# Optimization experiments

Measured on AMD Instinct MI355X. Metric: run time of the kernel, lower is better.

## Reference

```python
import jax, jax.numpy as jnp
import numpy as np

B, N, F_, H, K_IN, K = 2, 768, 128, 128, 2, 2
TAU = 0.66


def setup_inputs() -> dict:
    key = jax.random.key(0)
    ks = jax.random.split(key, 8)
    s = lambda fan: 1.0 / np.sqrt(fan)
    X = jax.random.normal(ks[0], (B, N, F_), jnp.float32)
    # edge_feat RezeroMLP: Linear(F,H) -> act -> Linear(H,H)
    ef_w1 = jax.random.normal(ks[1], (F_, H), jnp.float32) * s(F_)
    ef_b1 = jnp.zeros((H,), jnp.float32)
    ef_w2 = jax.random.normal(ks[2], (H, H), jnp.float32) * s(H)
    ef_b2 = jnp.zeros((H,), jnp.float32)
    # rezero gate (init 0 in module; use small nonzero so the branch is exercised)
    gate = jnp.asarray(0.1, jnp.float32)
    # score_mlp RezeroMLP: Linear(k_in,H) -> ReLU -> Linear(H,k)
    sm_w1 = jax.random.normal(ks[3], (K_IN, H), jnp.float32) * s(K_IN)
    sm_b1 = jnp.zeros((H,), jnp.float32)
    sm_w2 = jax.random.normal(ks[4], (H, K), jnp.float32) * s(H)
    sm_b2 = jnp.zeros((K,), jnp.float32)
    # pre-sampled standard Gumbel noise for gumbel_softmax
    u = jax.random.uniform(ks[5], (B, N, N, K), jnp.float32, minval=1e-6, maxval=1.0 - 1e-6)
    gumbel = -jnp.log(-jnp.log(u))
    return {"X": X, "ef_w1": ef_w1, "ef_b1": ef_b1, "ef_w2": ef_w2, "ef_b2": ef_b2,
            "gate": gate, "sm_w1": sm_w1, "sm_b1": sm_b1, "sm_w2": sm_w2, "sm_b2": sm_b2,
            "gumbel": gumbel}


def reference(X, ef_w1, ef_b1, ef_w2, ef_b2, gate, sm_w1, sm_b1, sm_w2, sm_b2, gumbel):
    # edge_feat MLP: [B,N,F] -> [B,N,H]
    feats = jax.nn.relu(X @ ef_w1 + ef_b1) @ ef_w2 + ef_b2
    D = H // K_IN
    Xact = feats.reshape(B, N, D, K_IN)
    Xskip = X.reshape(B, N, D, K_IN)  # feat_dim == hidden_dim, proj is None
    Xc = (Xskip + gate * Xact).transpose(0, 3, 1, 2)  # [B,k_in,N,D]
    # pairwise outer product ('prod' scoring): [B,N,N,k_in]
    prod = jnp.einsum('bkid,bkjd->bijk', Xc, Xc)
    # per-edge score MLP: k_in -> H -> k
    scores = jax.nn.relu(prod @ sm_w1 + sm_b1) @ sm_w2 + sm_b2  # [B,N,N,k]
    logits = scores - jnp.max(scores, axis=-1, keepdims=True)
    # gumbel-softmax, hard (straight-through)
    y_soft = jax.nn.softmax((logits + gumbel) / TAU, axis=-1)
    y_hard = jax.nn.one_hot(jnp.argmax(y_soft, axis=-1), K, dtype=y_soft.dtype)
    y = y_hard + y_soft - jax.lax.stop_gradient(y_soft)
    # A = y @ zo with zo = [0,1,...]: probability/one-hot mass of 'edge' states
    zo = jnp.ones((K,), y.dtype).at[0].set(0.0)
    A = y @ zo  # [B,N,N]
    # zero diagonal and symmetrize via upper triangle
    Au = jnp.triu(A, 1)
    return Au + jnp.swapaxes(Au, -1, -2)
```

## Files before the change

### kernel.cpp

```cpp
#include <hip/hip_runtime.h>

#define BB 2
#define NN 768
#define FF 128
#define HH 128
#define TS 32
#define ROWS 8

__global__ void pack_weights_kernel(const float* __restrict__ sm_w1,
                                    const float* __restrict__ sm_b1,
                                    const float* __restrict__ sm_w2,
                                    double* __restrict__ wpack) {
    int c = threadIdx.x;
    if (c < HH) {
        wpack[4 * c + 0] = (double)sm_w1[c];
        wpack[4 * c + 1] = (double)sm_w1[HH + c];
        wpack[4 * c + 2] = (double)sm_b1[c];
        wpack[4 * c + 3] = (double)sm_w2[2 * c + 1] - (double)sm_w2[2 * c + 0];
    }
}

__global__ __launch_bounds__(128)
void edgefeat_kernel(const float* __restrict__ X,
                     const float* __restrict__ w1, const float* __restrict__ b1,
                     const float* __restrict__ w2, const float* __restrict__ b2,
                     const float* __restrict__ gatep,
                     double* __restrict__ Xc) {
    __shared__ float  Xs[ROWS][FF];
    __shared__ double Hs[ROWS][HH];
    const int h = threadIdx.x;
    const int row0 = blockIdx.x * ROWS;
    for (int r = 0; r < ROWS; ++r) Xs[r][h] = X[(size_t)(row0 + r) * FF + h];
    __syncthreads();
    double acc[ROWS];
    double bb = (double)b1[h];
    for (int r = 0; r < ROWS; ++r) acc[r] = bb;
    for (int f = 0; f < FF; ++f) {
        double w = (double)w1[f * HH + h];
        for (int r = 0; r < ROWS; ++r) acc[r] = fma((double)Xs[r][f], w, acc[r]);
    }
    for (int r = 0; r < ROWS; ++r) Hs[r][h] = acc[r] > 0.0 ? acc[r] : 0.0;
    __syncthreads();
    bb = (double)b2[h];
    for (int r = 0; r < ROWS; ++r) acc[r] = bb;
    for (int c = 0; c < HH; ++c) {
        double w = (double)w2[c * HH + h];
        for (int r = 0; r < ROWS; ++r) acc[r] = fma(Hs[r][c], w, acc[r]);
    }
    const double gate = (double)gatep[0];
    const int k = h & 1, d = h >> 1;
    const int b = row0 / NN;
    const int i0 = row0 % NN;
    for (int r = 0; r < ROWS; ++r) {
        double v = (double)Xs[r][h] + gate * acc[r];
        Xc[(((size_t)(b * 2 + k)) * NN + (i0 + r)) * 64 + d] = v;
    }
}

__global__ __launch_bounds__(256, 2)
void edge_decide_kernel(const double* __restrict__ Xc,
                        const double* __restrict__ wpack,
                        const float* __restrict__ sm_b2,
                        const float* __restrict__ gumbel,
                        float* __restrict__ out) {
    const int ti = blockIdx.x, tj = blockIdx.y, b = blockIdx.z;
    if (tj < ti) return;
    __shared__ double Ai[2][TS][66];
    __shared__ double Aj[2][TS][66];
    __shared__ float  As[TS][TS + 1];
    const int tid = threadIdx.x;
    const int i0 = ti * TS, j0 = tj * TS;

    for (int q = 0; q < 8; ++q) {
        int flat = tid + 256 * q;
        int k  = flat >> 10;
        int r  = (flat >> 5) & 31;
        int dp = flat & 31;
        size_t base = ((size_t)(b * 2 + k)) * NN;
        double2 vi = *(const double2*)&Xc[(base + i0 + r) * 64 + 2 * dp];
        *(double2*)&Ai[k][r][2 * dp] = vi;
        double2 vj = *(const double2*)&Xc[(base + j0 + r) * 64 + 2 * dp];
        *(double2*)&Aj[k][r][2 * dp] = vj;
    }
    __syncthreads();

    const int rh = tid >> 4;
    const int ch = tid & 15;
    const int r0 = rh, r1 = rh + 16;
    const int c0 = 2 * ch, c1 = c0 + 1;

    double p000 = 0, p001 = 0, p010 = 0, p011 = 0;
    double p100 = 0, p101 = 0, p110 = 0, p111 = 0;
    for (int d2 = 0; d2 < 32; ++d2) {
        double2 a00 = *(const double2*)&Ai[0][r0][2 * d2];
        double2 a01 = *(const double2*)&Ai[0][r1][2 * d2];
        double2 a10 = *(const double2*)&Ai[1][r0][2 * d2];
        double2 a11 = *(const double2*)&Ai[1][r1][2 * d2];
        double2 b00 = *(const double2*)&Aj[0][c0][2 * d2];
        double2 b01 = *(const double2*)&Aj[0][c1][2 * d2];
        double2 b10 = *(const double2*)&Aj[1][c0][2 * d2];
        double2 b11 = *(const double2*)&Aj[1][c1][2 * d2];
        p000 = fma(a00.y, b00.y, fma(a00.x, b00.x, p000));
        p001 = fma(a00.y, b01.y, fma(a00.x, b01.x, p001));
        p010 = fma(a01.y, b00.y, fma(a01.x, b00.x, p010));
        p011 = fma(a01.y, b01.y, fma(a01.x, b01.x, p011));
        p100 = fma(a10.y, b10.y, fma(a10.x, b10.x, p100));
        p101 = fma(a10.y, b11.y, fma(a10.x, b11.x, p101));
        p110 = fma(a11.y, b10.y, fma(a11.x, b10.x, p110));
        p111 = fma(a11.y, b11.y, fma(a11.x, b11.x, p111));
    }

    const double bd = (double)sm_b2[1] - (double)sm_b2[0];
    float4 g0v = *(const float4*)&gumbel[(((size_t)b * NN + i0 + r0) * NN + j0 + c0) * 2];
    float4 g1v = *(const float4*)&gumbel[(((size_t)b * NN + i0 + r1) * NN + j0 + c0) * 2];
    double m00 = bd + ((double)g0v.y - (double)g0v.x);
    double m01 = bd + ((double)g0v.w - (double)g0v.z);
    double m10 = bd + ((double)g1v.y - (double)g1v.x);
    double m11 = bd + ((double)g1v.w - (double)g1v.z);

    for (int c = 0; c < HH; ++c) {
        double2 wab = *(const double2*)&wpack[4 * c];
        double2 wbw = *(const double2*)&wpack[4 * c + 2];
        double t;
        t = fma(p100, wab.y, fma(p000, wab.x, wbw.x)); t = fmax(t, 0.0); m00 = fma(t, wbw.y, m00);
        t = fma(p101, wab.y, fma(p001, wab.x, wbw.x)); t = fmax(t, 0.0); m01 = fma(t, wbw.y, m01);
        t = fma(p110, wab.y, fma(p010, wab.x, wbw.x)); t = fmax(t, 0.0); m10 = fma(t, wbw.y, m10);
        t = fma(p111, wab.y, fma(p011, wab.x, wbw.x)); t = fmax(t, 0.0); m11 = fma(t, wbw.y, m11);
    }

    float A00 = m00 > 0.0 ? 1.0f : 0.0f;
    float A01 = m01 > 0.0 ? 1.0f : 0.0f;
    float A10 = m10 > 0.0 ? 1.0f : 0.0f;
    float A11 = m11 > 0.0 ? 1.0f : 0.0f;

    As[r0][c0] = A00; As[r0][c1] = A01;
    As[r1][c0] = A10; As[r1][c1] = A11;
    __syncthreads();

    if (ti != tj) {
        *(float2*)&out[((size_t)b * NN + i0 + r0) * NN + j0 + c0] = make_float2(A00, A01);
        *(float2*)&out[((size_t)b * NN + i0 + r1) * NN + j0 + c0] = make_float2(A10, A11);
        float2 t0 = make_float2(As[c0][r0], As[c1][r0]);
        *(float2*)&out[((size_t)b * NN + j0 + r0) * NN + i0 + c0] = t0;
        float2 t1 = make_float2(As[c0][r1], As[c1][r1]);
        *(float2*)&out[((size_t)b * NN + j0 + r1) * NN + i0 + c0] = t1;
    } else {
        float v00 = (r0 < c0) ? As[r0][c0] : ((r0 > c0) ? As[c0][r0] : 0.0f);
        float v01 = (r0 < c1) ? As[r0][c1] : ((r0 > c1) ? As[c1][r0] : 0.0f);
        float v10 = (r1 < c0) ? As[r1][c0] : ((r1 > c0) ? As[c0][r1] : 0.0f);
        float v11 = (r1 < c1) ? As[r1][c1] : ((r1 > c1) ? As[c1][r1] : 0.0f);
        *(float2*)&out[((size_t)b * NN + i0 + r0) * NN + j0 + c0] = make_float2(v00, v01);
        *(float2*)&out[((size_t)b * NN + i0 + r1) * NN + j0 + c0] = make_float2(v10, v11);
    }
}

extern "C" void kernel_launch(void* const* d_in, const int* in_sizes, int n_in,
                              void* d_out, int out_size, void* d_ws, size_t ws_size,
                              hipStream_t stream) {
    const float* X      = (const float*)d_in[0];
    const float* ef_w1  = (const float*)d_in[1];
    const float* ef_b1  = (const float*)d_in[2];
    const float* ef_w2  = (const float*)d_in[3];
    const float* ef_b2  = (const float*)d_in[4];
    const float* gate   = (const float*)d_in[5];
    const float* sm_w1  = (const float*)d_in[6];
    const float* sm_b1  = (const float*)d_in[7];
    const float* sm_w2  = (const float*)d_in[8];
    const float* sm_b2  = (const float*)d_in[9];
    const float* gumbel = (const float*)d_in[10];
    float* out = (float*)d_out;

    double* Xc    = (double*)d_ws;
    double* wpack = Xc + (size_t)BB * 2 * NN * 64;

    pack_weights_kernel<<<1, 128, 0, stream>>>(sm_w1, sm_b1, sm_w2, wpack);
    edgefeat_kernel<<<BB * NN / ROWS, 128, 0, stream>>>(X, ef_w1, ef_b1, ef_w2, ef_b2, gate, Xc);
    dim3 grid(NN / TS, NN / TS, BB);
    edge_decide_kernel<<<grid, 256, 0, stream>>>(Xc, wpack, sm_b2, gumbel, out);
}
```

Measured before the change: 139.6 us.

## Decide edges in fp32 and repair near-threshold edges in fp64

The pairwise edge-decision kernel now computes dot products and the score MLP in fp32 instead of fp64. Edges whose margin falls within a small delta of zero are appended to a worklist through an atomic counter, and a separate repair kernel recomputes them in fp64. The weight packing is folded into the edge-feature kernel, and output writes are widened to float4. The aim is to avoid slow fp64 ALU throughput, at the cost of an extra kernel launch, atomic contention and the risk that the fixed delta misses sign flips.

```diff
diff --git a/kernel.cpp b/kernel.cpp
--- a/kernel.cpp
+++ b/kernel.cpp
@@ -5,152 +5,230 @@
 #define FF 128
 #define HH 128
 #define TS 32
-#define ROWS 8
-
-__global__ void pack_weights_kernel(const float* __restrict__ sm_w1,
-                                    const float* __restrict__ sm_b1,
-                                    const float* __restrict__ sm_w2,
-                                    double* __restrict__ wpack) {
-    int c = threadIdx.x;
-    if (c < HH) {
-        wpack[4 * c + 0] = (double)sm_w1[c];
-        wpack[4 * c + 1] = (double)sm_w1[HH + c];
-        wpack[4 * c + 2] = (double)sm_b1[c];
-        wpack[4 * c + 3] = (double)sm_w2[2 * c + 1] - (double)sm_w2[2 * c + 0];
-    }
-}
+#define ROWS 4
+#define PAD 68
+#define DELTA 0.02f
+#define WCAP (1u << 20)
 
 __global__ __launch_bounds__(128)
 void edgefeat_kernel(const float* __restrict__ X,
                      const float* __restrict__ w1, const float* __restrict__ b1,
                      const float* __restrict__ w2, const float* __restrict__ b2,
                      const float* __restrict__ gatep,
-                     double* __restrict__ Xc) {
+                     const float* __restrict__ sm_w1, const float* __restrict__ sm_b1,
+                     const float* __restrict__ sm_w2,
+                     double* __restrict__ Xc64, float* __restrict__ Xc32,
+                     double* __restrict__ wpack64, float* __restrict__ wpackf,
+                     unsigned* __restrict__ counter) {
     __shared__ float  Xs[ROWS][FF];
-    __shared__ double Hs[ROWS][HH];
+    __shared__ double Hs[ROWS][HH + 2];
     const int h = threadIdx.x;
     const int row0 = blockIdx.x * ROWS;
+
+    if (blockIdx.x == 0) {
+        double a  = (double)sm_w1[h];
+        double bb = (double)sm_w1[HH + h];
+        double be = (double)sm_b1[h];
+        double wd = (double)sm_w2[2 * h + 1] - (double)sm_w2[2 * h];
+        wpack64[4 * h + 0] = a;  wpack64[4 * h + 1] = bb;
+        wpack64[4 * h + 2] = be; wpack64[4 * h + 3] = wd;
+        wpackf[4 * h + 0] = (float)a;  wpackf[4 * h + 1] = (float)bb;
+        wpackf[4 * h + 2] = (float)be; wpackf[4 * h + 3] = (float)wd;
+        if (h == 0) *counter = 0u;
+    }
+
     for (int r = 0; r < ROWS; ++r) Xs[r][h] = X[(size_t)(row0 + r) * FF + h];
     __syncthreads();
+
     double acc[ROWS];
-    double bb = (double)b1[h];
-    for (int r = 0; r < ROWS; ++r) acc[r] = bb;
+    double bi = (double)b1[h];
+    for (int r = 0; r < ROWS; ++r) acc[r] = bi;
+#pragma unroll 4
     for (int f = 0; f < FF; ++f) {
         double w = (double)w1[f * HH + h];
         for (int r = 0; r < ROWS; ++r) acc[r] = fma((double)Xs[r][f], w, acc[r]);
     }
     for (int r = 0; r < ROWS; ++r) Hs[r][h] = acc[r] > 0.0 ? acc[r] : 0.0;
     __syncthreads();
-    bb = (double)b2[h];
-    for (int r = 0; r < ROWS; ++r) acc[r] = bb;
+
+    bi = (double)b2[h];
+    for (int r = 0; r < ROWS; ++r) acc[r] = bi;
+#pragma unroll 4
     for (int c = 0; c < HH; ++c) {
         double w = (double)w2[c * HH + h];
         for (int r = 0; r < ROWS; ++r) acc[r] = fma(Hs[r][c], w, acc[r]);
     }
+
     const double gate = (double)gatep[0];
     const int k = h & 1, d = h >> 1;
     const int b = row0 / NN;
     const int i0 = row0 % NN;
     for (int r = 0; r < ROWS; ++r) {
         double v = (double)Xs[r][h] + gate * acc[r];
-        Xc[(((size_t)(b * 2 + k)) * NN + (i0 + r)) * 64 + d] = v;
-    }
-}
-
-__global__ __launch_bounds__(256, 2)
-void edge_decide_kernel(const double* __restrict__ Xc,
-                        const double* __restrict__ wpack,
-                        const float* __restrict__ sm_b2,
-                        const float* __restrict__ gumbel,
-                        float* __restrict__ out) {
+        size_t idx = (((size_t)(b * 2 + k)) * NN + (i0 + r)) * 64 + d;
+        Xc64[idx] = v;
+        Xc32[idx] = (float)v;
+    }
+}
+
+__global__ __launch_bounds__(256)
+void decide32_kernel(const float* __restrict__ Xc32,
+                     const float* __restrict__ wpackf,
+                     const float* __restrict__ sm_b2,
+                     const float* __restrict__ gumbel,
+                     float* __restrict__ out,
+                     unsigned* __restrict__ counter,
+                     unsigned* __restrict__ worklist) {
     const int ti = blockIdx.x, tj = blockIdx.y, b = blockIdx.z;
     if (tj < ti) return;
-    __shared__ double Ai[2][TS][66];
-    __shared__ double Aj[2][TS][66];
-    __shared__ float  As[TS][TS + 1];
+    __shared__ float Ai[2][TS][PAD];
+    __shared__ float Aj[2][TS][PAD];
+    __shared__ float As[TS][36];
     const int tid = threadIdx.x;
     const int i0 = ti * TS, j0 = tj * TS;
 
-    for (int q = 0; q < 8; ++q) {
+    for (int q = 0; q < 4; ++q) {
         int flat = tid + 256 * q;
-        int k  = flat >> 10;
-        int r  = (flat >> 5) & 31;
-        int dp = flat & 31;
+        int k  = flat >> 9;
+        int r  = (flat >> 4) & 31;
+        int d4 = (flat & 15) * 4;
         size_t base = ((size_t)(b * 2 + k)) * NN;
-        double2 vi = *(const double2*)&Xc[(base + i0 + r) * 64 + 2 * dp];
-        *(double2*)&Ai[k][r][2 * dp] = vi;
-        double2 vj = *(const double2*)&Xc[(base + j0 + r) * 64 + 2 * dp];
-        *(double2*)&Aj[k][r][2 * dp] = vj;
+        float4 vi = *(const float4*)&Xc32[(base + i0 + r) * 64 + d4];
+        *(float4*)&Ai[k][r][d4] = vi;
+        float4 vj = *(const float4*)&Xc32[(base + j0 + r) * 64 + d4];
+        *(float4*)&Aj[k][r][d4] = vj;
     }
     __syncthreads();
 
     const int rh = tid >> 4;
     const int ch = tid & 15;
     const int r0 = rh, r1 = rh + 16;
-    const int c0 = 2 * ch, c1 = c0 + 1;
-
-    double p000 = 0, p001 = 0, p010 = 0, p011 = 0;
-    double p100 = 0, p101 = 0, p110 = 0, p111 = 0;
-    for (int d2 = 0; d2 < 32; ++d2) {
-        double2 a00 = *(const double2*)&Ai[0][r0][2 * d2];
-        double2 a01 = *(const double2*)&Ai[0][r1][2 * d2];
-        double2 a10 = *(const double2*)&Ai[1][r0][2 * d2];
-        double2 a11 = *(const double2*)&Ai[1][r1][2 * d2];
-        double2 b00 = *(const double2*)&Aj[0][c0][2 * d2];
-        double2 b01 = *(const double2*)&Aj[0][c1][2 * d2];
-        double2 b10 = *(const double2*)&Aj[1][c0][2 * d2];
-        double2 b11 = *(const double2*)&Aj[1][c1][2 * d2];
-        p000 = fma(a00.y, b00.y, fma(a00.x, b00.x, p000));
-        p001 = fma(a00.y, b01.y, fma(a00.x, b01.x, p001));
-        p010 = fma(a01.y, b00.y, fma(a01.x, b00.x, p010));
-        p011 = fma(a01.y, b01.y, fma(a01.x, b01.x, p011));
-        p100 = fma(a10.y, b10.y, fma(a10.x, b10.x, p100));
-        p101 = fma(a10.y, b11.y, fma(a10.x, b11.x, p101));
-        p110 = fma(a11.y, b10.y, fma(a11.x, b10.x, p110));
-        p111 = fma(a11.y, b11.y, fma(a11.x, b11.x, p111));
-    }
-
-    const double bd = (double)sm_b2[1] - (double)sm_b2[0];
-    float4 g0v = *(const float4*)&gumbel[(((size_t)b * NN + i0 + r0) * NN + j0 + c0) * 2];
-    float4 g1v = *(const float4*)&gumbel[(((size_t)b * NN + i0 + r1) * NN + j0 + c0) * 2];
-    double m00 = bd + ((double)g0v.y - (double)g0v.x);
-    double m01 = bd + ((double)g0v.w - (double)g0v.z);
-    double m10 = bd + ((double)g1v.y - (double)g1v.x);
-    double m11 = bd + ((double)g1v.w - (double)g1v.z);
-
+    const int c0 = ch, c1 = ch + 16;
+
+    float p000 = 0.f, p001 = 0.f, p010 = 0.f, p011 = 0.f;
+    float p100 = 0.f, p101 = 0.f, p110 = 0.f, p111 = 0.f;
+#pragma unroll
+    for (int d4 = 0; d4 < 64; d4 += 4) {
+        float4 a00 = *(const float4*)&Ai[0][r0][d4];
+        float4 a01 = *(const float4*)&Ai[0][r1][d4];
+        float4 a10 = *(const float4*)&Ai[1][r0][d4];
+        float4 a11 = *(const float4*)&Ai[1][r1][d4];
+        float4 b00 = *(const float4*)&Aj[0][c0][d4];
+        float4 b01 = *(const float4*)&Aj[0][c1][d4];
+        float4 b10 = *(const float4*)&Aj[1][c0][d4];
+        float4 b11 = *(const float4*)&Aj[1][c1][d4];
+        p000 += a00.x*b00.x + a00.y*b00.y + a00.z*b00.z + a00.w*b00.w;
+        p001 += a00.x*b01.x + a00.y*b01.y + a00.z*b01.z + a00.w*b01.w;
+        p010 += a01.x*b00.x + a01.y*b00.y + a01.z*b00.z + a01.w*b00.w;
+        p011 += a01.x*b01.x + a01.y*b01.y + a01.z*b01.z + a01.w*b01.w;
+        p100 += a10.x*b10.x + a10.y*b10.y + a10.z*b10.z + a10.w*b10.w;
+        p101 += a10.x*b11.x + a10.y*b11.y + a10.z*b11.z + a10.w*b11.w;
+        p110 += a11.x*b10.x + a11.y*b10.y + a11.z*b10.z + a11.w*b10.w;
+        p111 += a11.x*b11.x + a11.y*b11.y + a11.z*b11.z + a11.w*b11.w;
+    }
+
+    const float bd = sm_b2[1] - sm_b2[0];
+    const float* gbase = &gumbel[(((size_t)b * NN) * NN) * 2];
+    float2 g00 = *(const float2*)&gbase[(((size_t)(i0 + r0)) * NN + j0 + c0) * 2];
+    float2 g01 = *(const float2*)&gbase[(((size_t)(i0 + r0)) * NN + j0 + c1) * 2];
+    float2 g10 = *(const float2*)&gbase[(((size_t)(i0 + r1)) * NN + j0 + c0) * 2];
+    float2 g11 = *(const float2*)&gbase[(((size_t)(i0 + r1)) * NN + j0 + c1) * 2];
+    float m00 = bd + (g00.y - g00.x);
+    float m01 = bd + (g01.y - g01.x);
+    float m10 = bd + (g10.y - g10.x);
+    float m11 = bd + (g11.y - g11.x);
+
+#pragma unroll 8
     for (int c = 0; c < HH; ++c) {
-        double2 wab = *(const double2*)&wpack[4 * c];
-        double2 wbw = *(const double2*)&wpack[4 * c + 2];
-        double t;
-        t = fma(p100, wab.y, fma(p000, wab.x, wbw.x)); t = fmax(t, 0.0); m00 = fma(t, wbw.y, m00);
-        t = fma(p101, wab.y, fma(p001, wab.x, wbw.x)); t = fmax(t, 0.0); m01 = fma(t, wbw.y, m01);
-        t = fma(p110, wab.y, fma(p010, wab.x, wbw.x)); t = fmax(t, 0.0); m10 = fma(t, wbw.y, m10);
-        t = fma(p111, wab.y, fma(p011, wab.x, wbw.x)); t = fmax(t, 0.0); m11 = fma(t, wbw.y, m11);
-    }
-
-    float A00 = m00 > 0.0 ? 1.0f : 0.0f;
-    float A01 = m01 > 0.0 ? 1.0f : 0.0f;
-    float A10 = m10 > 0.0 ? 1.0f : 0.0f;
-    float A11 = m11 > 0.0 ? 1.0f : 0.0f;
-
-    As[r0][c0] = A00; As[r0][c1] = A01;
-    As[r1][c0] = A10; As[r1][c1] = A11;
-    __syncthreads();
-
-    if (ti != tj) {
-        *(float2*)&out[((size_t)b * NN + i0 + r0) * NN + j0 + c0] = make_float2(A00, A01);
-        *(float2*)&out[((size_t)b * NN + i0 + r1) * NN + j0 + c0] = make_float2(A10, A11);
-        float2 t0 = make_float2(As[c0][r0], As[c1][r0]);
-        *(float2*)&out[((size_t)b * NN + j0 + r0) * NN + i0 + c0] = t0;
-        float2 t1 = make_float2(As[c0][r1], As[c1][r1]);
-        *(float2*)&out[((size_t)b * NN + j0 + r1) * NN + i0 + c0] = t1;
+        float4 w = *(const float4*)&wpackf[4 * c];
+        float t;
+        t = fmaf(p100, w.y, fmaf(p000, w.x, w.z)); t = fmaxf(t, 0.f); m00 = fmaf(t, w.w, m00);
+        t = fmaf(p101, w.y, fmaf(p001, w.x, w.z)); t = fmaxf(t, 0.f); m01 = fmaf(t, w.w, m01);
+        t = fmaf(p110, w.y, fmaf(p010, w.x, w.z)); t = fmaxf(t, 0.f); m10 = fmaf(t, w.w, m10);
+        t = fmaf(p111, w.y, fmaf(p011, w.x, w.z)); t = fmaxf(t, 0.f); m11 = fmaf(t, w.w, m11);
+    }
+
+    {
+        int gi0 = i0 + r0, gi1 = i0 + r1, gj0 = j0 + c0, gj1 = j0 + c1;
+        float mm[4] = {m00, m01, m10, m11};
+        int ii[4] = {gi0, gi0, gi1, gi1};
+        int jj[4] = {gj0, gj1, gj0, gj1};
+        for (int e = 0; e < 4; ++e) {
+            if (jj[e] > ii[e] && fabsf(mm[e]) < DELTA) {
+                unsigned slot = atomicAdd(counter, 1u);
+                if (slot < WCAP)
+                    worklist[slot] = ((unsigned)(b * NN + ii[e])) * NN + (unsigned)jj[e];
+            }
+        }
+    }
+
+    As[r0][c0] = m00 > 0.f ? 1.f : 0.f;
+    As[r0][c1] = m01 > 0.f ? 1.f : 0.f;
+    As[r1][c0] = m10 > 0.f ? 1.f : 0.f;
+    As[r1][c1] = m11 > 0.f ? 1.f : 0.f;
+    __syncthreads();
+
+    const int r  = tid >> 3;
+    const int c4 = (tid & 7) * 4;
+    if (ti == tj) {
+        float4 v;
+        float* vp = (float*)&v;
+        for (int u = 0; u < 4; ++u) {
+            int c = c4 + u;
+            vp[u] = (r < c) ? As[r][c] : ((r > c) ? As[c][r] : 0.f);
+        }
+        *(float4*)&out[((size_t)b * NN + i0 + r) * NN + j0 + c4] = v;
     } else {
-        float v00 = (r0 < c0) ? As[r0][c0] : ((r0 > c0) ? As[c0][r0] : 0.0f);
-        float v01 = (r0 < c1) ? As[r0][c1] : ((r0 > c1) ? As[c1][r0] : 0.0f);
-        float v10 = (r1 < c0) ? As[r1][c0] : ((r1 > c0) ? As[c0][r1] : 0.0f);
-        float v11 = (r1 < c1) ? As[r1][c1] : ((r1 > c1) ? As[c1][r1] : 0.0f);
-        *(float2*)&out[((size_t)b * NN + i0 + r0) * NN + j0 + c0] = make_float2(v00, v01);
-        *(float2*)&out[((size_t)b * NN + i0 + r1) * NN + j0 + c0] = make_float2(v10, v11);
+        float4 v = *(const float4*)&As[r][c4];
+        *(float4*)&out[((size_t)b * NN + i0 + r) * NN + j0 + c4] = v;
+        float4 t;
+        float* tp = (float*)&t;
+        for (int u = 0; u < 4; ++u) tp[u] = As[c4 + u][r];
+        *(float4*)&out[((size_t)b * NN + j0 + r) * NN + i0 + c4] = t;
+    }
+}
+
+__global__ __launch_bounds__(64)
+void repair_kernel(const double* __restrict__ Xc64,
+                   const double* __restrict__ wpack64,
+                   const float* __restrict__ sm_b2,
+                   const float* __restrict__ gumbel,
+                   float* __restrict__ out,
+                   const unsigned* __restrict__ counter,
+                   const unsigned* __restrict__ worklist) {
+    unsigned n = *counter;
+    if (n > WCAP) n = WCAP;
+    for (unsigned t = blockIdx.x * blockDim.x + threadIdx.x; t < n;
+         t += gridDim.x * blockDim.x) {
+        unsigned e = worklist[t];
+        int j = e % NN;
+        unsigned rr = e / NN;
+        int i = rr % NN;
+        int b = rr / NN;
+        const double* xi0 = &Xc64[(((size_t)(b * 2 + 0)) * NN + i) * 64];
+        const double* xj0 = &Xc64[(((size_t)(b * 2 + 0)) * NN + j) * 64];
+        const double* xi1 = &Xc64[(((size_t)(b * 2 + 1)) * NN + i) * 64];
+        const double* xj1 = &Xc64[(((size_t)(b * 2 + 1)) * NN + j) * 64];
+        double p0a = 0, p0b = 0, p1a = 0, p1b = 0;
+        for (int d = 0; d < 64; d += 2) {
+            p0a = fma(xi0[d],     xj0[d],     p0a);
+            p0b = fma(xi0[d + 1], xj0[d + 1], p0b);
+            p1a = fma(xi1[d],     xj1[d],     p1a);
+            p1b = fma(xi1[d + 1], xj1[d + 1], p1b);
+        }
+        double p0 = p0a + p0b, p1 = p1a + p1b;
+        const float* g = &gumbel[(((size_t)b * NN + i) * NN + j) * 2];
+        double m = ((double)sm_b2[1] - (double)sm_b2[0]) + ((double)g[1] - (double)g[0]);
+        for (int c = 0; c < HH; ++c) {
+            double2 wab = *(const double2*)&wpack64[4 * c];
+            double2 wbw = *(const double2*)&wpack64[4 * c + 2];
+            double tt = fma(p1, wab.y, fma(p0, wab.x, wbw.x));
+            tt = fmax(tt, 0.0);
+            m = fma(tt, wbw.y, m);
+        }
+        float v = m > 0.0 ? 1.f : 0.f;
+        out[((size_t)b * NN + i) * NN + j] = v;
+        out[((size_t)b * NN + j) * NN + i] = v;
     }
 }
 
@@ -170,11 +248,19 @@
     const float* gumbel = (const float*)d_in[10];
     float* out = (float*)d_out;
 
-    double* Xc    = (double*)d_ws;
-    double* wpack = Xc + (size_t)BB * 2 * NN * 64;
-
-    pack_weights_kernel<<<1, 128, 0, stream>>>(sm_w1, sm_b1, sm_w2, wpack);
-    edgefeat_kernel<<<BB * NN / ROWS, 128, 0, stream>>>(X, ef_w1, ef_b1, ef_w2, ef_b2, gate, Xc);
+    double*   Xc64     = (double*)d_ws;
+    float*    Xc32     = (float*)(Xc64 + 196608);
+    double*   wpack64  = (double*)(Xc32 + 196608);
+    float*    wpackf   = (float*)(wpack64 + 512);
+    unsigned* counter  = (unsigned*)(wpackf + 512);
+    unsigned* worklist = counter + 4;
+
+    edgefeat_kernel<<<BB * NN / ROWS, 128, 0, stream>>>(
+        X, ef_w1, ef_b1, ef_w2, ef_b2, gate, sm_w1, sm_b1, sm_w2,
+        Xc64, Xc32, wpack64, wpackf, counter);
     dim3 grid(NN / TS, NN / TS, BB);
-    edge_decide_kernel<<<grid, 256, 0, stream>>>(Xc, wpack, sm_b2, gumbel, out);
-}
+    decide32_kernel<<<grid, 256, 0, stream>>>(Xc32, wpackf, sm_b2, gumbel, out,
+                                              counter, worklist);
+    repair_kernel<<<32, 64, 0, stream>>>(Xc64, wpack64, sm_b2, gumbel, out,
+                                         counter, worklist);
+}
```

Measured after the change: 160.1 us. +14.7%, slower.
